# Performance work log

Hardware: AMD Instinct MI355X
Metric: run time of the kernel (lower is better)

Reference implementation:

```python
import jax, jax.numpy as jnp
import numpy as np

N_NODES = 50000
N_EDGES = 600000
D = 128
H = 256

def _mlp(x, W1, b1, W2, b2):
    return jax.nn.relu(x @ W1 + b1) @ W2 + b2

def setup_inputs() -> dict:
    key = jax.random.key(0)
    ks = jax.random.split(key, 8)
    s = lambda fan_in: 1.0 / np.sqrt(fan_in)
    return {
        "node_feat": jax.random.normal(ks[0], (N_NODES, D), jnp.float32),
        "edge_feat": jax.random.normal(ks[1], (N_EDGES, D), jnp.float32),
        "senders": jax.random.randint(ks[2], (N_EDGES,), 0, N_NODES, jnp.int32),
        "receivers": jax.random.randint(ks[3], (N_EDGES,), 0, N_NODES, jnp.int32),
        "eW1": jax.random.normal(ks[4], (3 * D, H), jnp.float32) * s(3 * D),
        "eb1": jnp.zeros((H,), jnp.float32),
        "eW2": jax.random.normal(ks[5], (H, D), jnp.float32) * s(H),
        "eb2": jnp.zeros((D,), jnp.float32),
        "nW1": jax.random.normal(ks[6], (3 * D, H), jnp.float32) * s(3 * D),
        "nb1": jnp.zeros((H,), jnp.float32),
        "nW2": jax.random.normal(ks[7], (H, D), jnp.float32) * s(H),
        "nb2": jnp.zeros((D,), jnp.float32),
    }

def reference(node_feat, edge_feat, senders, receivers,
              eW1, eb1, eW2, eb2, nW1, nb1, nW2, nb2):
    # --- edge update: gather sender/receiver node features, MLP ---
    sent = node_feat[senders]        # [E, D]
    received = node_feat[receivers]  # [E, D]
    e_in = jnp.concatenate([edge_feat, sent, received], axis=-1)  # [E, 3D]
    new_edges = _mlp(e_in, eW1, eb1, eW2, eb2)  # [E, D]

    # --- node update: segment_sum aggregate edges sent by / received at node ---
    sent_agg = jax.ops.segment_sum(new_edges, senders, num_segments=N_NODES)
    recv_agg = jax.ops.segment_sum(new_edges, receivers, num_segments=N_NODES)
    n_in = jnp.concatenate([node_feat, sent_agg, recv_agg], axis=-1)  # [N, 3D]
    new_nodes = _mlp(n_in, nW1, nb1, nW2, nb2)  # [N, D]

    return new_nodes, new_edges
```

## Files before the change

kernel.cpp:

```cpp
#include <hip/hip_runtime.h>


typedef unsigned short ushort_t;
typedef __attribute__((ext_vector_type(8))) short bf16x8;
typedef __attribute__((ext_vector_type(4))) float f32x4;

#define MFMA16(a, b, c) __builtin_amdgcn_mfma_f32_16x16x32_bf16(a, b, c, 0, 0, 0)

__device__ __forceinline__ ushort_t f2bf(float f) {
    unsigned int u = __builtin_bit_cast(unsigned int, f);
    u += 0x7fffu + ((u >> 16) & 1u);
    return (ushort_t)(u >> 16);
}

__global__ void pack_all(const float* __restrict__ eW1, const float* __restrict__ eW2,
                         const float* __restrict__ nW1, const float* __restrict__ nW2,
                         ushort_t* __restrict__ eW1p, ushort_t* __restrict__ eW2p,
                         ushort_t* __restrict__ nW1p, ushort_t* __restrict__ nW2p) {
    int idx = blockIdx.x * 256 + threadIdx.x;
    const float* W; ushort_t* Wp; int N, local;
    if (idx < 98304)       { W = eW1; Wp = eW1p; N = 256; local = idx; }
    else if (idx < 131072) { W = eW2; Wp = eW2p; N = 128; local = idx - 98304; }
    else if (idx < 229376) { W = nW1; Wp = nW1p; N = 256; local = idx - 131072; }
    else                   { W = nW2; Wp = nW2p; N = 128; local = idx - 229376; }
    int k = local / N;
    int n = local - k * N;
    Wp[((size_t)((k >> 3) * N + n)) * 8 + (k & 7)] = f2bf(W[(size_t)k * N + n]);
}

#define APITCH 392
#define HPITCH 72

__global__ __launch_bounds__(256, 2)
void edge_kernel(const float* __restrict__ node_feat, const float* __restrict__ edge_feat,
                 const int* __restrict__ senders, const int* __restrict__ receivers,
                 const ushort_t* __restrict__ W1p, const float* __restrict__ b1,
                 const ushort_t* __restrict__ W2p, const float* __restrict__ b2,
                 float* __restrict__ new_edges, float* __restrict__ sent_agg,
                 float* __restrict__ recv_agg) {
    __shared__ ushort_t Alds[64 * APITCH];
    __shared__ ushort_t Wlds[8192];
    __shared__ ushort_t Hlds[64 * HPITCH];

    const int tid = threadIdx.x;
    const int ebase = blockIdx.x * 64;

    for (int t = tid; t < 6144; t += 256) {
        int row = t / 96;
        int p   = t - row * 96;
        int e   = ebase + row;
        int k0  = p * 4;
        const float* src;
        if (p < 32)      src = edge_feat + (size_t)e * 128 + k0;
        else if (p < 64) src = node_feat + (size_t)senders[e] * 128 + (k0 - 128);
        else             src = node_feat + (size_t)receivers[e] * 128 + (k0 - 256);
        float4 v = *(const float4*)src;
        ushort4 w;
        w.x = f2bf(v.x); w.y = f2bf(v.y); w.z = f2bf(v.z); w.w = f2bf(v.w);
        *(ushort4*)&Alds[row * APITCH + k0] = w;
    }
    __syncthreads();

    const int wv   = tid >> 6;
    const int lane = tid & 63;
    const int lrow = lane & 15;
    const int lq   = lane >> 4;
    const int arow = wv * 16 + lrow;

    f32x4 acc2[8];
#pragma unroll
    for (int i = 0; i < 8; i++) acc2[i] = (f32x4){0.f, 0.f, 0.f, 0.f};

#pragma unroll
    for (int s = 0; s < 4; s++) {
        const int sbase = s * 64;
        f32x4 acc1[4];
#pragma unroll
        for (int i = 0; i < 4; i++) acc1[i] = (f32x4){0.f, 0.f, 0.f, 0.f};

#pragma unroll
        for (int kc = 0; kc < 3; kc++) {
            const int kcb = kc * 128;
            for (int u = tid; u < 1024; u += 256) {
                int kq16 = u >> 6;
                int n    = u & 63;
                *(uint4*)&Wlds[u * 8] =
                    *(const uint4*)&W1p[(size_t)(((kcb >> 3) + kq16) * 256 + sbase + n) * 8];
            }
            __syncthreads();
#pragma unroll
            for (int kt = 0; kt < 4; kt++) {
                bf16x8 a = *(const bf16x8*)&Alds[arow * APITCH + kcb + kt * 32 + lq * 8];
#pragma unroll
                for (int nt = 0; nt < 4; nt++) {
                    bf16x8 b = *(const bf16x8*)&Wlds[((kt * 4 + lq) * 64 + nt * 16 + lrow) * 8];
                    acc1[nt] = MFMA16(a, b, acc1[nt]);
                }
            }
            __syncthreads();
        }

#pragma unroll
        for (int nt = 0; nt < 4; nt++) {
            float bb = b1[sbase + nt * 16 + lrow];
#pragma unroll
            for (int rg = 0; rg < 4; rg++) {
                int row = wv * 16 + lq * 4 + rg;
                float v = acc1[nt][rg] + bb;
                v = v > 0.f ? v : 0.f;
                Hlds[row * HPITCH + nt * 16 + lrow] = f2bf(v);
            }
        }
        __syncthreads();

        for (int u = tid; u < 1024; u += 256) {
            int kq16 = u >> 7;
            int n    = u & 127;
            *(uint4*)&Wlds[u * 8] = *(const uint4*)&W2p[(size_t)((s * 8 + kq16) * 128 + n) * 8];
        }
        __syncthreads();

#pragma unroll
        for (int kt = 0; kt < 2; kt++) {
            bf16x8 a = *(const bf16x8*)&Hlds[arow * HPITCH + kt * 32 + lq * 8];
#pragma unroll
            for (int nt = 0; nt < 8; nt++) {
                bf16x8 b = *(const bf16x8*)&Wlds[((kt * 4 + lq) * 128 + nt * 16 + lrow) * 8];
                acc2[nt] = MFMA16(a, b, acc2[nt]);
            }
        }
        __syncthreads();
    }

    float bv[8];
#pragma unroll
    for (int nt = 0; nt < 8; nt++) bv[nt] = b2[nt * 16 + lrow];
#pragma unroll
    for (int rg = 0; rg < 4; rg++) {
        int row = wv * 16 + lq * 4 + rg;
        int e   = ebase + row;
        int si  = senders[e];
        int ri  = receivers[e];
        float* er = new_edges + (size_t)e * 128;
        float* sa = sent_agg + (size_t)si * 128;
        float* ra = recv_agg + (size_t)ri * 128;
#pragma unroll
        for (int nt = 0; nt < 8; nt++) {
            int col = nt * 16 + lrow;
            float v = acc2[nt][rg] + bv[nt];
            er[col] = v;
            atomicAdd(sa + col, v);
            atomicAdd(ra + col, v);
        }
    }
}

__global__ __launch_bounds__(256, 2)
void node_kernel(const float* __restrict__ node_feat, const float* __restrict__ sent_agg,
                 const float* __restrict__ recv_agg,
                 const ushort_t* __restrict__ W1p, const float* __restrict__ b1,
                 const ushort_t* __restrict__ W2p, const float* __restrict__ b2,
                 float* __restrict__ new_nodes) {
    __shared__ ushort_t Alds[64 * APITCH];
    __shared__ ushort_t Wlds[8192];
    __shared__ ushort_t Hlds[64 * HPITCH];

    const int tid = threadIdx.x;
    const int nbase = blockIdx.x * 64;

    for (int t = tid; t < 6144; t += 256) {
        int row = t / 96;
        int p   = t - row * 96;
        int n   = nbase + row;
        int k0  = p * 4;
        float4 v = (float4){0.f, 0.f, 0.f, 0.f};
        if (n < 50000) {
            const float* src;
            if (p < 32)      src = node_feat + (size_t)n * 128 + k0;
            else if (p < 64) src = sent_agg + (size_t)n * 128 + (k0 - 128);
            else             src = recv_agg + (size_t)n * 128 + (k0 - 256);
            v = *(const float4*)src;
        }
        ushort4 w;
        w.x = f2bf(v.x); w.y = f2bf(v.y); w.z = f2bf(v.z); w.w = f2bf(v.w);
        *(ushort4*)&Alds[row * APITCH + k0] = w;
    }
    __syncthreads();

    const int wv   = tid >> 6;
    const int lane = tid & 63;
    const int lrow = lane & 15;
    const int lq   = lane >> 4;
    const int arow = wv * 16 + lrow;

    f32x4 acc2[8];
#pragma unroll
    for (int i = 0; i < 8; i++) acc2[i] = (f32x4){0.f, 0.f, 0.f, 0.f};

#pragma unroll
    for (int s = 0; s < 4; s++) {
        const int sbase = s * 64;
        f32x4 acc1[4];
#pragma unroll
        for (int i = 0; i < 4; i++) acc1[i] = (f32x4){0.f, 0.f, 0.f, 0.f};

#pragma unroll
        for (int kc = 0; kc < 3; kc++) {
            const int kcb = kc * 128;
            for (int u = tid; u < 1024; u += 256) {
                int kq16 = u >> 6;
                int n    = u & 63;
                *(uint4*)&Wlds[u * 8] =
                    *(const uint4*)&W1p[(size_t)(((kcb >> 3) + kq16) * 256 + sbase + n) * 8];
            }
            __syncthreads();
#pragma unroll
            for (int kt = 0; kt < 4; kt++) {
                bf16x8 a = *(const bf16x8*)&Alds[arow * APITCH + kcb + kt * 32 + lq * 8];
#pragma unroll
                for (int nt = 0; nt < 4; nt++) {
                    bf16x8 b = *(const bf16x8*)&Wlds[((kt * 4 + lq) * 64 + nt * 16 + lrow) * 8];
                    acc1[nt] = MFMA16(a, b, acc1[nt]);
                }
            }
            __syncthreads();
        }

#pragma unroll
        for (int nt = 0; nt < 4; nt++) {
            float bb = b1[sbase + nt * 16 + lrow];
#pragma unroll
            for (int rg = 0; rg < 4; rg++) {
                int row = wv * 16 + lq * 4 + rg;
                float v = acc1[nt][rg] + bb;
                v = v > 0.f ? v : 0.f;
                Hlds[row * HPITCH + nt * 16 + lrow] = f2bf(v);
            }
        }
        __syncthreads();

        for (int u = tid; u < 1024; u += 256) {
            int kq16 = u >> 7;
            int n    = u & 127;
            *(uint4*)&Wlds[u * 8] = *(const uint4*)&W2p[(size_t)((s * 8 + kq16) * 128 + n) * 8];
        }
        __syncthreads();

#pragma unroll
        for (int kt = 0; kt < 2; kt++) {
            bf16x8 a = *(const bf16x8*)&Hlds[arow * HPITCH + kt * 32 + lq * 8];
#pragma unroll
            for (int nt = 0; nt < 8; nt++) {
                bf16x8 b = *(const bf16x8*)&Wlds[((kt * 4 + lq) * 128 + nt * 16 + lrow) * 8];
                acc2[nt] = MFMA16(a, b, acc2[nt]);
            }
        }
        __syncthreads();
    }

    float bv[8];
#pragma unroll
    for (int nt = 0; nt < 8; nt++) bv[nt] = b2[nt * 16 + lrow];
#pragma unroll
    for (int rg = 0; rg < 4; rg++) {
        int row = wv * 16 + lq * 4 + rg;
        int n   = nbase + row;
        if (n < 50000) {
            float* out = new_nodes + (size_t)n * 128;
#pragma unroll
            for (int nt = 0; nt < 8; nt++) {
                int col = nt * 16 + lrow;
                out[col] = acc2[nt][rg] + bv[nt];
            }
        }
    }
}

extern "C" void kernel_launch(void* const* d_in, const int* in_sizes, int n_in,
                              void* d_out, int out_size, void* d_ws, size_t ws_size,
                              hipStream_t stream) {
    const float* node_feat = (const float*)d_in[0];
    const float* edge_feat = (const float*)d_in[1];
    const int*   senders   = (const int*)d_in[2];
    const int*   receivers = (const int*)d_in[3];
    const float* eW1 = (const float*)d_in[4];
    const float* eb1 = (const float*)d_in[5];
    const float* eW2 = (const float*)d_in[6];
    const float* eb2 = (const float*)d_in[7];
    const float* nW1 = (const float*)d_in[8];
    const float* nb1 = (const float*)d_in[9];
    const float* nW2 = (const float*)d_in[10];
    const float* nb2 = (const float*)d_in[11];

    float* new_nodes = (float*)d_out;
    float* new_edges = (float*)d_out + 6400000;

    float* sent_agg = (float*)d_ws;
    float* recv_agg = sent_agg + 6400000;
    ushort_t* eW1p = (ushort_t*)((char*)d_ws + 51200000);
    ushort_t* eW2p = eW1p + 98304;
    ushort_t* nW1p = eW2p + 32768;
    ushort_t* nW2p = nW1p + 98304;

    hipMemsetAsync(d_ws, 0, 51200000, stream);
    pack_all<<<1024, 256, 0, stream>>>(eW1, eW2, nW1, nW2, eW1p, eW2p, nW1p, nW2p);
    edge_kernel<<<9375, 256, 0, stream>>>(node_feat, edge_feat, senders, receivers,
                                          eW1p, eb1, eW2p, eb2,
                                          new_edges, sent_agg, recv_agg);
    node_kernel<<<782, 256, 0, stream>>>(node_feat, sent_agg, recv_agg,
                                         nW1p, nb1, nW2p, nb2, new_nodes);
}
```

Before: 1.776 ms.

## Replace float atomic scatter with CSR gather-based segment sums in node kernel

Result: no change. 1.801 ms (+1.4%).

```diff
diff --git a/kernel.cpp b/kernel.cpp
--- a/kernel.cpp
+++ b/kernel.cpp
@@ -28,6 +28,69 @@
     Wp[((size_t)((k >> 3) * N + n)) * 8 + (k & 7)] = f2bf(W[(size_t)k * N + n]);
 }
 
+__global__ void hist_kernel(const int* __restrict__ senders, const int* __restrict__ receivers,
+                            int* __restrict__ cnt_s, int* __restrict__ cnt_r) {
+    int e = blockIdx.x * 256 + threadIdx.x;
+    if (e < 600000) {
+        atomicAdd(&cnt_s[senders[e]], 1);
+        atomicAdd(&cnt_r[receivers[e]], 1);
+    }
+}
+
+__device__ __forceinline__ int wave_incl_scan(int v, int lane) {
+#pragma unroll
+    for (int d = 1; d < 64; d <<= 1) {
+        int t = __shfl_up(v, d, 64);
+        if (lane >= d) v += t;
+    }
+    return v;
+}
+
+__global__ void scan_kernel(const int* __restrict__ cnt, int* __restrict__ off,
+                            int* __restrict__ cur) {
+    const int n = 50000;
+    cnt += blockIdx.x * n; off += blockIdx.x * n; cur += blockIdx.x * n;
+    const int tid  = threadIdx.x;
+    const int lane = tid & 63;
+    const int wv   = tid >> 6;
+    __shared__ int wsum[16];
+    int carry = 0;
+    for (int base = 0; base < n; base += 1024) {
+        int i = base + tid;
+        int v = (i < n) ? cnt[i] : 0;
+        int incl = wave_incl_scan(v, lane);
+        if (lane == 63) wsum[wv] = incl;
+        __syncthreads();
+        if (wv == 0 && lane < 16) {
+            int s = wsum[lane];
+#pragma unroll
+            for (int d = 1; d < 16; d <<= 1) {
+                int t = __shfl_up(s, d, 64);
+                if (lane >= d) s += t;
+            }
+            wsum[lane] = s;
+        }
+        __syncthreads();
+        int wbase = (wv == 0) ? 0 : wsum[wv - 1];
+        int excl  = carry + wbase + incl - v;
+        if (i < n) { off[i] = excl; cur[i] = excl; }
+        carry += wsum[15];
+        __syncthreads();
+    }
+}
+
+__global__ void scatter_kernel(const int* __restrict__ senders, const int* __restrict__ receivers,
+                               int* __restrict__ cur_s, int* __restrict__ cur_r,
+                               int* __restrict__ idx_s, int* __restrict__ idx_r) {
+    int e = blockIdx.x * 256 + threadIdx.x;
+    if (e < 600000) {
+        int p = atomicAdd(&cur_s[senders[e]], 1);
+        idx_s[p] = e;
+        int q = atomicAdd(&cur_r[receivers[e]], 1);
+        idx_r[q] = e;
+    }
+}
+
 #define APITCH 392
 #define HPITCH 72
 
@@ -36,8 +99,7 @@
                  const int* __restrict__ senders, const int* __restrict__ receivers,
                  const ushort_t* __restrict__ W1p, const float* __restrict__ b1,
                  const ushort_t* __restrict__ W2p, const float* __restrict__ b2,
-                 float* __restrict__ new_edges, float* __restrict__ sent_agg,
-                 float* __restrict__ recv_agg) {
+                 float* __restrict__ new_edges) {
     __shared__ ushort_t Alds[64 * APITCH];
     __shared__ ushort_t Wlds[8192];
     __shared__ ushort_t Hlds[64 * HPITCH];
@@ -138,26 +200,20 @@
 #pragma unroll
     for (int rg = 0; rg < 4; rg++) {
         int row = wv * 16 + lq * 4 + rg;
-        int e   = ebase + row;
-        int si  = senders[e];
-        int ri  = receivers[e];
-        float* er = new_edges + (size_t)e * 128;
-        float* sa = sent_agg + (size_t)si * 128;
-        float* ra = recv_agg + (size_t)ri * 128;
+        float* er = new_edges + (size_t)(ebase + row) * 128;
 #pragma unroll
         for (int nt = 0; nt < 8; nt++) {
-            int col = nt * 16 + lrow;
-            float v = acc2[nt][rg] + bv[nt];
-            er[col] = v;
-            atomicAdd(sa + col, v);
-            atomicAdd(ra + col, v);
+            er[nt * 16 + lrow] = acc2[nt][rg] + bv[nt];
         }
     }
 }
 
 __global__ __launch_bounds__(256, 2)
-void node_kernel(const float* __restrict__ node_feat, const float* __restrict__ sent_agg,
-                 const float* __restrict__ recv_agg,
+void node_kernel(const float* __restrict__ node_feat, const float* __restrict__ new_edges,
+                 const int* __restrict__ off_s, const int* __restrict__ cnt_s,
+                 const int* __restrict__ idx_s,
+                 const int* __restrict__ off_r, const int* __restrict__ cnt_r,
+                 const int* __restrict__ idx_r,
                  const ushort_t* __restrict__ W1p, const float* __restrict__ b1,
                  const ushort_t* __restrict__ W2p, const float* __restrict__ b2,
                  float* __restrict__ new_nodes) {
@@ -167,23 +223,63 @@
 
     const int tid = threadIdx.x;
     const int nbase = blockIdx.x * 64;
-
-    for (int t = tid; t < 6144; t += 256) {
-        int row = t / 96;
-        int p   = t - row * 96;
-        int n   = nbase + row;
-        int k0  = p * 4;
-        float4 v = (float4){0.f, 0.f, 0.f, 0.f};
-        if (n < 50000) {
-            const float* src;
-            if (p < 32)      src = node_feat + (size_t)n * 128 + k0;
-            else if (p < 64) src = sent_agg + (size_t)n * 128 + (k0 - 128);
-            else             src = recv_agg + (size_t)n * 128 + (k0 - 256);
-            v = *(const float4*)src;
-        }
-        ushort4 w;
-        w.x = f2bf(v.x); w.y = f2bf(v.y); w.z = f2bf(v.z); w.w = f2bf(v.w);
-        *(ushort4*)&Alds[row * APITCH + k0] = w;
+    const int nrow  = tid >> 2;
+    const int tq    = tid & 3;
+    const int n     = nbase + nrow;
+    const int cbase = tq * 32;
+
+    if (n < 50000) {
+        const float* nf = node_feat + (size_t)n * 128 + cbase;
+#pragma unroll
+        for (int i = 0; i < 8; i++) {
+            f32x4 v = *(const f32x4*)(nf + i * 4);
+            ushort4 w;
+            w.x = f2bf(v[0]); w.y = f2bf(v[1]); w.z = f2bf(v[2]); w.w = f2bf(v[3]);
+            *(ushort4*)&Alds[nrow * APITCH + cbase + i * 4] = w;
+        }
+        f32x4 acc[8];
+#pragma unroll
+        for (int i = 0; i < 8; i++) acc[i] = (f32x4){0.f, 0.f, 0.f, 0.f};
+        {
+            int j0 = off_s[n], j1 = j0 + cnt_s[n];
+            for (int j = j0; j < j1; j++) {
+                const float* er = new_edges + (size_t)idx_s[j] * 128 + cbase;
+#pragma unroll
+                for (int i = 0; i < 8; i++) acc[i] += *(const f32x4*)(er + i * 4);
+            }
+        }
+#pragma unroll
+        for (int i = 0; i < 8; i++) {
+            ushort4 w;
+            w.x = f2bf(acc[i][0]); w.y = f2bf(acc[i][1]);
+            w.z = f2bf(acc[i][2]); w.w = f2bf(acc[i][3]);
+            *(ushort4*)&Alds[nrow * APITCH + 128 + cbase + i * 4] = w;
+        }
+#pragma unroll
+        for (int i = 0; i < 8; i++) acc[i] = (f32x4){0.f, 0.f, 0.f, 0.f};
+        {
+            int j0 = off_r[n], j1 = j0 + cnt_r[n];
+            for (int j = j0; j < j1; j++) {
+                const float* er = new_edges + (size_t)idx_r[j] * 128 + cbase;
+#pragma unroll
+                for (int i = 0; i < 8; i++) acc[i] += *(const f32x4*)(er + i * 4);
+            }
+        }
+#pragma unroll
+        for (int i = 0; i < 8; i++) {
+            ushort4 w;
+            w.x = f2bf(acc[i][0]); w.y = f2bf(acc[i][1]);
+            w.z = f2bf(acc[i][2]); w.w = f2bf(acc[i][3]);
+            *(ushort4*)&Alds[nrow * APITCH + 256 + cbase + i * 4] = w;
+        }
+    } else {
+        ushort4 z = {0, 0, 0, 0};
+#pragma unroll
+        for (int i = 0; i < 8; i++) {
+            *(ushort4*)&Alds[nrow * APITCH + cbase + i * 4] = z;
+            *(ushort4*)&Alds[nrow * APITCH + 128 + cbase + i * 4] = z;
+            *(ushort4*)&Alds[nrow * APITCH + 256 + cbase + i * 4] = z;
+        }
     }
     __syncthreads();
 
@@ -209,9 +305,9 @@
             const int kcb = kc * 128;
             for (int u = tid; u < 1024; u += 256) {
                 int kq16 = u >> 6;
-                int n    = u & 63;
+                int nn   = u & 63;
                 *(uint4*)&Wlds[u * 8] =
-                    *(const uint4*)&W1p[(size_t)(((kcb >> 3) + kq16) * 256 + sbase + n) * 8];
+                    *(const uint4*)&W1p[(size_t)(((kcb >> 3) + kq16) * 256 + sbase + nn) * 8];
             }
             __syncthreads();
 #pragma unroll
@@ -241,8 +337,8 @@
 
         for (int u = tid; u < 1024; u += 256) {
             int kq16 = u >> 7;
-            int n    = u & 127;
-            *(uint4*)&Wlds[u * 8] = *(const uint4*)&W2p[(size_t)((s * 8 + kq16) * 128 + n) * 8];
+            int nn   = u & 127;
+            *(uint4*)&Wlds[u * 8] = *(const uint4*)&W2p[(size_t)((s * 8 + kq16) * 128 + nn) * 8];
         }
         __syncthreads();
 
@@ -264,13 +360,12 @@
 #pragma unroll
     for (int rg = 0; rg < 4; rg++) {
         int row = wv * 16 + lq * 4 + rg;
-        int n   = nbase + row;
-        if (n < 50000) {
-            float* out = new_nodes + (size_t)n * 128;
+        int nn  = nbase + row;
+        if (nn < 50000) {
+            float* out = new_nodes + (size_t)nn * 128;
 #pragma unroll
             for (int nt = 0; nt < 8; nt++) {
-                int col = nt * 16 + lrow;
-                out[col] = acc2[nt][rg] + bv[nt];
+                out[nt * 16 + lrow] = acc2[nt][rg] + bv[nt];
             }
         }
     }
@@ -295,18 +390,27 @@
     float* new_nodes = (float*)d_out;
     float* new_edges = (float*)d_out + 6400000;
 
-    float* sent_agg = (float*)d_ws;
-    float* recv_agg = sent_agg + 6400000;
-    ushort_t* eW1p = (ushort_t*)((char*)d_ws + 51200000);
+    int* cnt_s = (int*)d_ws;
+    int* cnt_r = cnt_s + 50000;
+    int* off_s = cnt_s + 100000;
+    int* off_r = cnt_s + 150000;
+    int* cur_s = cnt_s + 200000;
+    int* cur_r = cnt_s + 250000;
+    int* idx_s = cnt_s + 300000;
+    int* idx_r = cnt_s + 900000;
+    ushort_t* eW1p = (ushort_t*)((char*)d_ws + 6000000);
     ushort_t* eW2p = eW1p + 98304;
     ushort_t* nW1p = eW2p + 32768;
     ushort_t* nW2p = nW1p + 98304;
 
-    hipMemsetAsync(d_ws, 0, 51200000, stream);
+    hipMemsetAsync(d_ws, 0, 400000, stream);
     pack_all<<<1024, 256, 0, stream>>>(eW1, eW2, nW1, nW2, eW1p, eW2p, nW1p, nW2p);
+    hist_kernel<<<2344, 256, 0, stream>>>(senders, receivers, cnt_s, cnt_r);
+    scan_kernel<<<2, 1024, 0, stream>>>(cnt_s, off_s, cur_s);
+    scatter_kernel<<<2344, 256, 0, stream>>>(senders, receivers, cur_s, cur_r, idx_s, idx_r);
     edge_kernel<<<9375, 256, 0, stream>>>(node_feat, edge_feat, senders, receivers,
-                                          eW1p, eb1, eW2p, eb2,
-                                          new_edges, sent_agg, recv_agg);
-    node_kernel<<<782, 256, 0, stream>>>(node_feat, sent_agg, recv_agg,
+                                          eW1p, eb1, eW2p, eb2, new_edges);
+    node_kernel<<<782, 256, 0, stream>>>(node_feat, new_edges,
+                                         off_s, cnt_s, idx_s, off_r, cnt_r, idx_r,
                                          nW1p, nb1, nW2p, nb2, new_nodes);
 }
```
